# Kernel optimization log

Measured on AMD Instinct MI355X. Metric: run time of the kernel, lower is better.

## Reference

```python
import jax, jax.numpy as jnp
import numpy as np

B, S, H = 1, 1024, 2048
NH, NKV, HD = 32, 4, 128
E, K, I = 32, 8, 768
EPS = 1e-06
ROPE_BASE = 1e6


def rmsnorm(x, w, eps=EPS):
    xf = x.astype(jnp.float32)
    var = jnp.mean(xf * xf, axis=-1, keepdims=True)
    return w * (xf * jax.lax.rsqrt(var + eps)).astype(x.dtype)


def apply_rope(x, cos, sin):
    # x: [B,S,N,HD]; cos/sin: [S,HD//2]; interleaved (llama-style) pair rotation
    xr = x.reshape(*x.shape[:-1], HD // 2, 2)
    x0, x1 = xr[..., 0], xr[..., 1]
    c = cos[None, :, None, :]
    s = sin[None, :, None, :]
    o0 = x0 * c - x1 * s
    o1 = x0 * s + x1 * c
    return jnp.stack([o0, o1], axis=-1).reshape(x.shape)


def setup_inputs() -> dict:
    key = jax.random.key(0)
    ks = jax.random.split(key, 16)
    hidden_states = jax.random.normal(ks[0], (B, S, H), dtype=jnp.float32)
    # RoPE angles: positions * inv_freq  -> [S, HD//2]
    inv_freq = 1.0 / (ROPE_BASE ** (np.arange(0, HD, 2, dtype=np.float32) / HD))
    position_embeddings = jnp.asarray(np.arange(S, dtype=np.float32)[:, None] * inv_freq[None, :])
    # causal additive mask [1,1,S,S]
    causal = jnp.tril(jnp.ones((S, S), dtype=bool))
    attention_mask = jnp.where(causal, 0.0, -1e9).astype(jnp.float32)[None, None]
    w = 0.02
    params = {
        'ln1_w': jnp.ones((H,), jnp.float32),
        'ln2_w': jnp.ones((H,), jnp.float32),
        'q_w': w * jax.random.normal(ks[1], (H, NH * HD), jnp.float32),
        'k_w': w * jax.random.normal(ks[2], (H, NKV * HD), jnp.float32),
        'v_w': w * jax.random.normal(ks[3], (H, NKV * HD), jnp.float32),
        'o_w': w * jax.random.normal(ks[4], (NH * HD, H), jnp.float32),
        'qn_w': jnp.ones((HD,), jnp.float32),
        'kn_w': jnp.ones((HD,), jnp.float32),
        'gate_w': w * jax.random.normal(ks[5], (H, E), jnp.float32),
        'wg': w * jax.random.normal(ks[6], (E, H, I), jnp.float32),
        'wu': w * jax.random.normal(ks[7], (E, H, I), jnp.float32),
        'wd': w * jax.random.normal(ks[8], (E, I, H), jnp.float32),
    }
    return {'hidden_states': hidden_states, 'position_embeddings': position_embeddings,
            'attention_mask': attention_mask, 'start_pos': 0, **params}


def reference(hidden_states, position_embeddings, attention_mask, start_pos,
              ln1_w, ln2_w, q_w, k_w, v_w, o_w, qn_w, kn_w, gate_w, wg, wu, wd):
    x = hidden_states  # [B,S,H]
    # --- attention ---
    h = rmsnorm(x, ln1_w)
    q = rmsnorm((h @ q_w).reshape(B, S, NH, HD), qn_w)
    k = rmsnorm((h @ k_w).reshape(B, S, NKV, HD), kn_w)
    v = (h @ v_w).reshape(B, S, NKV, HD)
    cos, sin = jnp.cos(position_embeddings), jnp.sin(position_embeddings)
    q = apply_rope(q, cos, sin)
    k = apply_rope(k, cos, sin)
    q = q.transpose(0, 2, 1, 3)  # [B,NH,S,HD]
    k = jnp.repeat(k.transpose(0, 2, 1, 3), NH // NKV, axis=1)
    v = jnp.repeat(v.transpose(0, 2, 1, 3), NH // NKV, axis=1)
    scores = jnp.einsum('bhqd,bhkd->bhqk', q, k) * (HD ** -0.5) + attention_mask
    attn = jax.nn.softmax(scores, axis=-1)
    o = jnp.einsum('bhqk,bhkd->bhqd', attn, v).transpose(0, 2, 1, 3).reshape(B, S, NH * HD)
    x = x + o @ o_w
    # --- MoE ---
    h = rmsnorm(x, ln2_w).reshape(B * S, H)  # [T,H]
    probs = jax.nn.softmax((h @ gate_w).astype(jnp.float32), axis=-1)
    rw, sel = jax.lax.top_k(probs, K)  # [T,K]
    rw = rw / jnp.sum(rw, axis=-1, keepdims=True)  # norm_topk_prob
    T = B * S
    # dense combine weights [T,E]; zero for unselected experts (same math as loop)
    wte = jnp.zeros((T, E), jnp.float32).at[jnp.arange(T)[:, None], sel].add(rw).astype(h.dtype)
    g = jnp.einsum('th,ehi->tei', h, wg)
    u = jnp.einsum('th,ehi->tei', h, wu)
    act = jax.nn.silu(g) * u  # [T,E,I]
    moe = jnp.einsum('te,tei,eih->th', wte, act, wd)
    return x + moe.reshape(B, S, H)
```

## Files before the change

kernel.cpp:

```cpp
#include <hip/hip_runtime.h>
#include <hip/hip_bf16.h>

#define S_ 1024
#define H_ 2048
#define NH_ 32
#define NKV_ 4
#define HD_ 128
#define NE_ 32
#define TOPK_ 8
#define I_ 768
#define EPS_ 1e-6f
#define QS_ 5120
#define BK2 32
#define NPAR 4

typedef __bf16 bf16_t;
typedef __bf16 bf16x4v __attribute__((ext_vector_type(4)));
typedef __bf16 bf16x8 __attribute__((ext_vector_type(8)));
typedef float f32x4 __attribute__((ext_vector_type(4)));
typedef float f32x16 __attribute__((ext_vector_type(16)));
typedef unsigned short u16_t;
typedef unsigned int uint2v __attribute__((ext_vector_type(2)));
typedef unsigned int uint4v __attribute__((ext_vector_type(4)));

static __device__ __forceinline__ u16_t f2u(float x) {
  return __builtin_bit_cast(u16_t, (__bf16)x);
}
static __device__ __forceinline__ float u2f(u16_t u) {
  return (float)__builtin_bit_cast(__bf16, u);
}

static __device__ __forceinline__ void gload16(const bf16_t* g, bf16_t* l) {
  __builtin_amdgcn_global_load_lds(
      (const __attribute__((address_space(1))) unsigned int*)g,
      (__attribute__((address_space(3))) unsigned int*)l, 16, 0, 0);
}

template <bool WF32>
__global__ __launch_bounds__(256) void rmsnorm2_k(const float* __restrict__ x,
                                                  const float* __restrict__ w,
                                                  float* __restrict__ outf,
                                                  bf16_t* __restrict__ outb) {
  int r = blockIdx.x, tid = threadIdx.x;
  const float* xr = x + (size_t)r * H_;
  f32x4 a = *(const f32x4*)(xr + tid * 8);
  f32x4 b = *(const f32x4*)(xr + tid * 8 + 4);
  float ss = 0.f;
#pragma unroll
  for (int i = 0; i < 4; ++i) ss += a[i] * a[i] + b[i] * b[i];
#pragma unroll
  for (int m = 1; m < 64; m <<= 1) ss += __shfl_xor(ss, m);
  __shared__ float wsum[4];
  if ((tid & 63) == 0) wsum[tid >> 6] = ss;
  __syncthreads();
  ss = wsum[0] + wsum[1] + wsum[2] + wsum[3];
  float inv = rsqrtf(ss * (1.0f / H_) + EPS_);
  f32x4 w0 = *(const f32x4*)(w + tid * 8);
  f32x4 w1 = *(const f32x4*)(w + tid * 8 + 4);
  f32x4 o0, o1;
#pragma unroll
  for (int i = 0; i < 4; ++i) { o0[i] = a[i] * inv * w0[i]; o1[i] = b[i] * inv * w1[i]; }
  if constexpr (WF32) {
    *(f32x4*)(outf + (size_t)r * H_ + tid * 8) = o0;
    *(f32x4*)(outf + (size_t)r * H_ + tid * 8 + 4) = o1;
  }
  bf16x8 ob;
#pragma unroll
  for (int i = 0; i < 4; ++i) { ob[i] = (__bf16)o0[i]; ob[i + 4] = (__bf16)o1[i]; }
  *(bf16x8*)(outb + (size_t)r * H_ + tid * 8) = ob;
}

__global__ __launch_bounds__(256) void transp2_k(const float* __restrict__ in,
                                                 bf16_t* __restrict__ out, int R, int C) {
  __shared__ float tile[64][65];
  size_t zin = (size_t)blockIdx.z * R * C;
  int tx = threadIdx.x & 15, ty = threadIdx.x >> 4;
  int r0 = blockIdx.y * 64, c0 = blockIdx.x * 64;
#pragma unroll
  for (int i = 0; i < 4; ++i) {
    f32x4 v = *(const f32x4*)(in + zin + (size_t)(r0 + ty + i * 16) * C + c0 + tx * 4);
    tile[ty + i * 16][tx * 4 + 0] = v[0];
    tile[ty + i * 16][tx * 4 + 1] = v[1];
    tile[ty + i * 16][tx * 4 + 2] = v[2];
    tile[ty + i * 16][tx * 4 + 3] = v[3];
  }
  __syncthreads();
#pragma unroll
  for (int i = 0; i < 4; ++i) {
    int oc = ty + i * 16;
    bf16x4v o;
#pragma unroll
    for (int j = 0; j < 4; ++j) o[j] = (bf16_t)tile[tx * 4 + j][oc];
    *(bf16x4v*)(out + zin + (size_t)(c0 + oc) * R + r0 + tx * 4) = o;
  }
}

template <int BMT, int BNT, int WM, int WN, typename TC, bool RESID>
__global__ __launch_bounds__(512) void gemmd_k(
    const bf16_t* __restrict__ A, const bf16_t* __restrict__ Bt,
    const float* __restrict__ resid, TC* __restrict__ C, int M, int N, int K) {
  constexpr int MI = BMT / WM / 16;
  constexpr int NI = BNT / WN / 16;
  constexpr int ALW = BMT / 16 / 8;
  constexpr int NBL = BNT / 16;
  static_assert(NBL <= 8, "B wave loads");
  __shared__ __align__(16) bf16_t As[2][BMT][BK2];
  __shared__ __align__(16) bf16_t Bs[2][BNT][BK2];
  int tid = threadIdx.x, lane = tid & 63, w = tid >> 6;
  int m0 = blockIdx.x * BMT, n0 = blockIdx.y * BNT;
  int srow = lane >> 2;
  int schunk = ((lane & 3) ^ ((lane >> 3) & 3)) * 8;
  const bf16_t* asrc[ALW];
#pragma unroll
  for (int i = 0; i < ALW; ++i) {
    int r = (w * ALW + i) * 16 + srow;
    asrc[i] = A + (size_t)(m0 + r) * K + schunk;
  }
  bool hasB = (w < NBL);
  int brow = w * 16;
  const bf16_t* bsrc = hasB ? Bt + (size_t)(n0 + brow + srow) * K + schunk : nullptr;

  int fr = lane & 15, g = lane >> 4;
  int rk = (g ^ ((fr >> 1) & 3)) * 8;
  int wm = w / WN, wn = w % WN;
  int rbase0 = wm * (BMT / WM), cbase0 = wn * (BNT / WN);
  f32x4 acc[MI][NI] = {};
  int NT = K / BK2;
  {
#pragma unroll
    for (int i = 0; i < ALW; ++i) gload16(asrc[i], &As[0][(w * ALW + i) * 16][0]);
    if (hasB) gload16(bsrc, &Bs[0][brow][0]);
  }
  __syncthreads();
  int cur = 0;
  for (int t = 0; t < NT; ++t) {
    if (t + 1 < NT) {
      int ko = (t + 1) * BK2;
#pragma unroll
      for (int i = 0; i < ALW; ++i) gload16(asrc[i] + ko, &As[cur ^ 1][(w * ALW + i) * 16][0]);
      if (hasB) gload16(bsrc + ko, &Bs[cur ^ 1][brow][0]);
    }
    bf16x8 af[MI], bf[NI];
#pragma unroll
    for (int i = 0; i < MI; ++i) af[i] = *(const bf16x8*)&As[cur][rbase0 + i * 16 + fr][rk];
#pragma unroll
    for (int i = 0; i < NI; ++i) bf[i] = *(const bf16x8*)&Bs[cur][cbase0 + i * 16 + fr][rk];
#pragma unroll
    for (int mi = 0; mi < MI; ++mi)
#pragma unroll
      for (int ni = 0; ni < NI; ++ni)
        acc[mi][ni] = __builtin_amdgcn_mfma_f32_16x16x32_bf16(af[mi], bf[ni], acc[mi][ni], 0, 0, 0);
    __syncthreads();
    cur ^= 1;
  }
  int rbase = g * 4;
#pragma unroll
  for (int mi = 0; mi < MI; ++mi)
#pragma unroll
    for (int ni = 0; ni < NI; ++ni)
#pragma unroll
      for (int r = 0; r < 4; ++r) {
        int gi = m0 + rbase0 + mi * 16 + rbase + r;
        int gc = n0 + cbase0 + ni * 16 + fr;
        float v = acc[mi][ni][r];
        if constexpr (RESID) v += resid[(size_t)gi * N + gc];
        C[(size_t)gi * N + gc] = (TC)v;
      }
}

template <int BMT, int BNT, int WM, int WN, typename TC, bool GATHER, bool SCALE, bool DUAL>
__global__ __launch_bounds__(512) void gemme_k(
    const bf16_t* __restrict__ A, const bf16_t* __restrict__ B1g,
    const bf16_t* __restrict__ B2g, TC* __restrict__ C, bf16_t* __restrict__ act,
    const float* __restrict__ wlist, const int* __restrict__ counts,
    const int* __restrict__ offsets, const int* __restrict__ toklist,
    const int* __restrict__ mslots, const int* __restrict__ meta,
    int* __restrict__ qhead, int NTN, int N, int K) {
  constexpr int MI = BMT / WM / 16;
  constexpr int NI = BNT / WN / 16;
  constexpr int BNTT = BNT * (DUAL ? 2 : 1);
  constexpr int ALW = BMT / 16 / 8;
  constexpr int NBL = BNTT / 16;
  static_assert(NBL <= 8, "B wave loads");
  __shared__ __align__(16) bf16_t As[2][BMT][BK2];
  __shared__ __align__(16) bf16_t Bs[2][BNTT][BK2];
  __shared__ int s_w;
  int tid = threadIdx.x, lane = tid & 63, w = tid >> 6;
  int srow = lane >> 2;
  int schunk = ((lane & 3) ^ ((lane >> 3) & 3)) * 8;
  int fr = lane & 15, g = lane >> 4;
  int rk = (g ^ ((fr >> 1) & 3)) * 8;
  int wm = w / WN, wn = w % WN;
  int rbase0 = wm * (BMT / WM), cbase0 = wn * (BNT / WN);
  int total = meta[0] * NTN;
  for (;;) {
    if (tid == 0) s_w = atomicAdd(qhead, 1);
    __syncthreads();
    int wk = s_w;
    if (wk >= total) return;
    int ms = mslots[wk / NTN];
    int n0 = (wk % NTN) * BNT;
    int e = ms >> 8, m0 = (ms & 255) * BMT;
    int cnt = counts[e], off = offsets[e];
    size_t bs = (size_t)K * N;
    const bf16_t* B1 = B1g + (size_t)e * bs;
    const bf16_t* B2 = DUAL ? (B2g + (size_t)e * bs) : nullptr;
    const bf16_t* asrc[ALW];
#pragma unroll
    for (int i = 0; i < ALW; ++i) {
      int r = (w * ALW + i) * 16 + srow;
      int gr = min(m0 + r, cnt - 1);
      size_t grow;
      if constexpr (GATHER) grow = (size_t)toklist[e * S_ + gr];
      else grow = (size_t)(off + gr);
      asrc[i] = A + grow * (size_t)K + schunk;
    }
    bool hasB = (w < NBL);
    const bf16_t* bsrc = nullptr;
    int brow = w * 16;
    if (hasB) {
      const bf16_t* Bb = (brow < BNT) ? B1 : B2;
      int rr = (brow < BNT) ? brow : brow - BNT;
      bsrc = Bb + (size_t)(n0 + rr + srow) * K + schunk;
    }
    f32x4 acc1[MI][NI] = {};
    f32x4 acc2[DUAL ? MI : 1][DUAL ? NI : 1] = {};
    int NT = K / BK2;
    {
#pragma unroll
      for (int i = 0; i < ALW; ++i) gload16(asrc[i], &As[0][(w * ALW + i) * 16][0]);
      if (hasB) gload16(bsrc, &Bs[0][brow][0]);
    }
    __syncthreads();
    int cur = 0;
    for (int t = 0; t < NT; ++t) {
      if (t + 1 < NT) {
        int ko = (t + 1) * BK2;
#pragma unroll
        for (int i = 0; i < ALW; ++i) gload16(asrc[i] + ko, &As[cur ^ 1][(w * ALW + i) * 16][0]);
        if (hasB) gload16(bsrc + ko, &Bs[cur ^ 1][brow][0]);
      }
      bf16x8 af[MI], b1f[NI], b2f[DUAL ? NI : 1];
#pragma unroll
      for (int i = 0; i < MI; ++i) af[i] = *(const bf16x8*)&As[cur][rbase0 + i * 16 + fr][rk];
#pragma unroll
      for (int i = 0; i < NI; ++i) b1f[i] = *(const bf16x8*)&Bs[cur][cbase0 + i * 16 + fr][rk];
      if constexpr (DUAL) {
#pragma unroll
        for (int i = 0; i < NI; ++i) b2f[i] = *(const bf16x8*)&Bs[cur][BNT + cbase0 + i * 16 + fr][rk];
      }
#pragma unroll
      for (int mi = 0; mi < MI; ++mi)
#pragma unroll
        for (int ni = 0; ni < NI; ++ni) {
          acc1[mi][ni] = __builtin_amdgcn_mfma_f32_16x16x32_bf16(af[mi], b1f[ni], acc1[mi][ni], 0, 0, 0);
          if constexpr (DUAL)
            acc2[mi][ni] = __builtin_amdgcn_mfma_f32_16x16x32_bf16(af[mi], b2f[ni], acc2[mi][ni], 0, 0, 0);
        }
      __syncthreads();
      cur ^= 1;
    }
    int rbase = g * 4;
#pragma unroll
    for (int mi = 0; mi < MI; ++mi)
#pragma unroll
      for (int ni = 0; ni < NI; ++ni)
#pragma unroll
        for (int r = 0; r < 4; ++r) {
          int lr = rbase0 + mi * 16 + rbase + r;
          int gi = m0 + lr;
          if (gi >= cnt) continue;
          int gc = n0 + cbase0 + ni * 16 + fr;
          if constexpr (DUAL) {
            float gv = acc1[mi][ni][r], uv = acc2[mi][ni][r];
            float sig = 1.0f / (1.0f + __expf(-gv));
            act[(size_t)(off + gi) * N + gc] = (bf16_t)(gv * sig * uv);
          } else {
            float v = acc1[mi][ni][r];
            if constexpr (SCALE) v *= wlist[(size_t)e * S_ + gi];
            C[(size_t)(off + gi) * N + gc] = (TC)v;
          }
        }
  }
}

__global__ __launch_bounds__(64) void qkpack_k(const float* __restrict__ qkv,
                                               const float* __restrict__ qn,
                                               const float* __restrict__ kn,
                                               const float* __restrict__ pe,
                                               bf16_t* __restrict__ Q2,
                                               bf16_t* __restrict__ K2) {
  int s = blockIdx.x, hh = blockIdx.y, lane = threadIdx.x;
  const float* ptr;
  const float* w;
  if (hh < NH_) { ptr = qkv + (size_t)s * QS_ + hh * HD_; w = qn; }
  else          { ptr = qkv + (size_t)s * QS_ + NH_ * HD_ + (hh - NH_) * HD_; w = kn; }
  float x0 = ptr[2 * lane], x1 = ptr[2 * lane + 1];
  float ss = x0 * x0 + x1 * x1;
#pragma unroll
  for (int m = 1; m < 64; m <<= 1) ss += __shfl_xor(ss, m);
  float inv = rsqrtf(ss * (1.0f / HD_) + EPS_);
  x0 = x0 * inv * w[2 * lane];
  x1 = x1 * inv * w[2 * lane + 1];
  float ang = pe[(size_t)s * (HD_ / 2) + lane];
  float sn, cs;
  sincosf(ang, &sn, &cs);
  float r0 = x0 * cs - x1 * sn;
  float r1 = x0 * sn + x1 * cs;
  if (hh < NH_) {
    const float scale = 0.08838834764831845f;
    float a = r0 * scale, b = r1 * scale;
    u16_t h0 = f2u(a), h1 = f2u(b);
    unsigned hw = (unsigned)h0 | ((unsigned)h1 << 16);
    unsigned lw = (unsigned)f2u(a - u2f(h0)) | ((unsigned)f2u(b - u2f(h1)) << 16);
    unsigned* base = (unsigned*)(Q2 + ((size_t)s * NH_ + hh) * 256);
    base[lane] = hw;
    base[64 + lane] = lw;
  } else {
    u16_t h0 = f2u(r0), h1 = f2u(r1);
    unsigned hw = (unsigned)h0 | ((unsigned)h1 << 16);
    unsigned lw = (unsigned)f2u(r0 - u2f(h0)) | ((unsigned)f2u(r1 - u2f(h1)) << 16);
    int j = lane >> 2, off = (2 * lane) & 7;
    unsigned* base = (unsigned*)(K2 + ((size_t)(hh - NH_) * S_ + s) * 256);
    base[(((j) ^ (s & 31)) * 8 + off) >> 1] = hw;
    base[(((16 + j) ^ (s & 31)) * 8 + off) >> 1] = lw;
  }
}

__global__ __launch_bounds__(256) void vpack_k(const float* __restrict__ qkv,
                                               bf16_t* __restrict__ V2T) {
  int t = blockIdx.x, kvh = blockIdx.y;
  int kv0 = t * 64;
  bf16_t* dst = V2T + (size_t)(kvh * 16 + t) * 128 * 128;
  const float* vbase = qkv + NH_ * HD_ + NKV_ * HD_ + kvh * HD_;
#pragma unroll
  for (int i = 0; i < 4; ++i) {
    int flat = threadIdx.x + i * 256;
    int kvp = flat >> 5, d4 = (flat & 31) * 4;
    const float* r0 = vbase + (size_t)(kv0 + 2 * kvp) * QS_ + d4;
    const float* r1 = r0 + QS_;
    f32x4 a = *(const f32x4*)r0;
    f32x4 b = *(const f32x4*)r1;
    int kvg = (2 * kvp) >> 3, sub = (2 * kvp) & 7;
#pragma unroll
    for (int e = 0; e < 4; ++e) {
      int d = d4 + e;
      int fsw = (d ^ (d >> 4)) & 15;
      u16_t ha = f2u(a[e]), hb = f2u(b[e]);
      unsigned hw = (unsigned)ha | ((unsigned)hb << 16);
      unsigned lw = (unsigned)f2u(a[e] - u2f(ha)) | ((unsigned)f2u(b[e] - u2f(hb)) << 16);
      unsigned* dd = (unsigned*)(dst + d * 128);
      dd[((kvg ^ fsw) * 8 + sub) >> 1] = hw;
      dd[(((8 + kvg) ^ fsw) * 8 + sub) >> 1] = lw;
    }
  }
}

#define AKV 64
__global__ __launch_bounds__(512, 4) void attn5_k(const bf16_t* __restrict__ Q2,
                                                  const bf16_t* __restrict__ K2,
                                                  const bf16_t* __restrict__ V2T,
                                                  float* __restrict__ Op,
                                                  float* __restrict__ mlp) {
  int q0 = blockIdx.x * 32;
  int kvh = blockIdx.y;
  int par = blockIdx.z;
  int tid = threadIdx.x, lane = tid & 63, w = tid >> 6;
  int g = lane >> 5, c32 = lane & 31;
  int h = kvh * 8 + w;
  int qrow = q0 + c32;
  int last_t = (q0 + 31) >> 6;
  float2* mlv = (float2*)mlp;
  if (par > last_t) {
    if (g == 0) {
      float2 v2; v2.x = -3.0e38f; v2.y = 0.f;
      mlv[((size_t)par * S_ + qrow) * NH_ + h] = v2;
    }
    return;
  }
  __shared__ __align__(16) u16_t Kl[AKV * 256];
  __shared__ __align__(16) u16_t Vl[128 * 128];

  bf16x8 qh[8], ql[8];
  {
    const bf16_t* qp2 = Q2 + ((size_t)qrow * NH_ + h) * 256;
#pragma unroll
    for (int ks = 0; ks < 8; ++ks) {
      qh[ks] = *(const bf16x8*)(qp2 + g * 8 + ks * 16);
      ql[ks] = *(const bf16x8*)(qp2 + 128 + g * 8 + ks * 16);
    }
  }

  f32x16 accO[4] = {};
  float m = -3.0e38f, l = 0.f;

  for (int t = par; t <= last_t; t += NPAR) {
    int kv0 = t * AKV;
    __syncthreads();
    {
      const bf16_t* ksrc = K2 + ((size_t)kvh * S_ + kv0) * 256;
#pragma unroll
      for (int i = 0; i < 4; ++i) {
        int cbase = w * 64 + i * 512;
        gload16(ksrc + (size_t)(cbase + lane) * 8, (bf16_t*)&Kl[cbase * 8]);
      }
    }
    {
      const bf16_t* vsrc = V2T + (size_t)(kvh * 16 + t) * 128 * 128;
#pragma unroll
      for (int i = 0; i < 4; ++i) {
        int cbase = w * 64 + i * 512;
        gload16(vsrc + (size_t)(cbase + lane) * 8, (bf16_t*)&Vl[cbase * 8]);
      }
    }
    __syncthreads();

    f32x16 accS[2] = {};
#pragma unroll
    for (int ks = 0; ks < 8; ++ks) {
      int db = g * 8 + ks * 16;
#pragma unroll
      for (int mf = 0; mf < 2; ++mf) {
        int kvr = c32 + mf * 32;
        bf16x8 ah = *(const bf16x8*)&Kl[kvr * 256 + (((db >> 3)) ^ c32) * 8];
        bf16x8 al = *(const bf16x8*)&Kl[kvr * 256 + ((16 + (db >> 3)) ^ c32) * 8];
        accS[mf] = __builtin_amdgcn_mfma_f32_32x32x16_bf16(ah, qh[ks], accS[mf], 0, 0, 0);
        accS[mf] = __builtin_amdgcn_mfma_f32_32x32x16_bf16(ah, ql[ks], accS[mf], 0, 0, 0);
        accS[mf] = __builtin_amdgcn_mfma_f32_32x32x16_bf16(al, qh[ks], accS[mf], 0, 0, 0);
      }
    }
    float p[2][16];
    float tmax = -3.0e38f;
#pragma unroll
    for (int mf = 0; mf < 2; ++mf)
#pragma unroll
      for (int r = 0; r < 16; ++r) {
        int kvg = kv0 + mf * 32 + (r & 3) + 8 * (r >> 2) + 4 * g;
        float s = (kvg <= qrow) ? accS[mf][r] : -3.0e38f;
        p[mf][r] = s;
        tmax = fmaxf(tmax, s);
      }
    tmax = fmaxf(tmax, __shfl_xor(tmax, 32));
    float mn = fmaxf(m, tmax);
    float sc = __expf(m - mn);
    float ts = 0.f;
#pragma unroll
    for (int mf = 0; mf < 2; ++mf)
#pragma unroll
      for (int r = 0; r < 16; ++r) {
        float e = __expf(p[mf][r] - mn);
        p[mf][r] = e;
        ts += e;
      }
    ts += __shfl_xor(ts, 32);
    l = l * sc + ts;
    m = mn;
#pragma unroll
    for (int r = 0; r < 16; ++r) {
      int row16 = (r & 3) + 8 * (r >> 2) + 4 * g;
      float scr = __shfl(sc, row16);
#pragma unroll
      for (int nf = 0; nf < 4; ++nf) accO[nf][r] *= scr;
    }
#pragma unroll
    for (int ks = 0; ks < 4; ++ks) {
      int k1 = ks & 1, mf = ks >> 1;
      unsigned Lh[4], Ll[4];
#pragma unroll
      for (int i = 0; i < 4; ++i) {
        float a = p[mf][8 * k1 + 2 * i], b = p[mf][8 * k1 + 2 * i + 1];
        u16_t ha = f2u(a), hb = f2u(b);
        Lh[i] = (unsigned)ha | ((unsigned)hb << 16);
        Ll[i] = (unsigned)f2u(a - u2f(ha)) | ((unsigned)f2u(b - u2f(hb)) << 16);
      }
      unsigned Xh[4], Xl[4];
#pragma unroll
      for (int i = 0; i < 4; ++i) {
        Xh[i] = (unsigned)__shfl_xor((int)Lh[i], 32);
        Xl[i] = (unsigned)__shfl_xor((int)Ll[i], 32);
      }
      uint4v fh, fl;
      fh[0] = g ? Xh[2] : Lh[0]; fh[1] = g ? Xh[3] : Lh[1];
      fh[2] = g ? Lh[2] : Xh[0]; fh[3] = g ? Lh[3] : Xh[1];
      fl[0] = g ? Xl[2] : Ll[0]; fl[1] = g ? Xl[3] : Ll[1];
      fl[2] = g ? Ll[2] : Xl[0]; fl[3] = g ? Ll[3] : Xl[1];
      bf16x8 pH = __builtin_bit_cast(bf16x8, fh);
      bf16x8 pL = __builtin_bit_cast(bf16x8, fl);
      int kvb = g * 8 + ks * 16;
#pragma unroll
      for (int nf = 0; nf < 4; ++nf) {
        int d = c32 + nf * 32;
        int fsw = (d ^ (d >> 4)) & 15;
        bf16x8 vh = *(const bf16x8*)&Vl[d * 128 + (((kvb >> 3)) ^ fsw) * 8];
        bf16x8 vl = *(const bf16x8*)&Vl[d * 128 + ((8 + (kvb >> 3)) ^ fsw) * 8];
        accO[nf] = __builtin_amdgcn_mfma_f32_32x32x16_bf16(pH, vh, accO[nf], 0, 0, 0);
        accO[nf] = __builtin_amdgcn_mfma_f32_32x32x16_bf16(pH, vl, accO[nf], 0, 0, 0);
        accO[nf] = __builtin_amdgcn_mfma_f32_32x32x16_bf16(pL, vh, accO[nf], 0, 0, 0);
      }
    }
  }
#pragma unroll
  for (int r = 0; r < 16; ++r) {
    int row16 = (r & 3) + 8 * (r >> 2) + 4 * g;
    int orow = q0 + row16;
#pragma unroll
    for (int nf = 0; nf < 4; ++nf)
      __builtin_nontemporal_store(
          accO[nf][r], &Op[(((size_t)par * S_ + orow) * NH_ + h) * HD_ + nf * 32 + c32]);
  }
  if (g == 0) {
    float2 v2; v2.x = m; v2.y = l;
    mlv[((size_t)par * S_ + qrow) * NH_ + h] = v2;
  }
}

__global__ __launch_bounds__(128) void attnmerge_k(const float* __restrict__ Op,
                                                   const float* __restrict__ mlp,
                                                   bf16_t* __restrict__ o) {
  int row = blockIdx.x, h = blockIdx.y, d = threadIdx.x;
  const float2* mlv = (const float2*)mlp;
  float mm[NPAR], ll[NPAR];
  float M = -3.0e38f;
#pragma unroll
  for (int p = 0; p < NPAR; ++p) {
    float2 v2 = mlv[((size_t)p * S_ + row) * NH_ + h];
    mm[p] = v2.x; ll[p] = v2.y;
    M = fmaxf(M, mm[p]);
  }
  float acc = 0.f, L = 0.f;
#pragma unroll
  for (int p = 0; p < NPAR; ++p) {
    if (ll[p] == 0.f) continue;
    float wp = __expf(mm[p] - M);
    acc += wp * __builtin_nontemporal_load(
                    &Op[(((size_t)p * S_ + row) * NH_ + h) * HD_ + d]);
    L += wp * ll[p];
  }
  o[((size_t)row * NH_ + h) * HD_ + d] = (bf16_t)(acc / L);
}

__global__ __launch_bounds__(256) void router2_k(const float* __restrict__ h2,
                                                 const float* __restrict__ gw,
                                                 int* __restrict__ sel,
                                                 float* __restrict__ wsel) {
  int t = blockIdx.x, tid = threadIdx.x;
  int e = tid & 31, grp = tid >> 5;
  float acc = 0.f;
  for (int kk = grp; kk < H_; kk += 8)
    acc += h2[(size_t)t * H_ + kk] * gw[(size_t)kk * NE_ + e];
  __shared__ float part[8][32];
  part[grp][e] = acc;
  __syncthreads();
  if (tid < 64) {
    int lane = tid;
    float lg = -3.0e38f;
    if (lane < 32) {
      lg = 0.f;
      for (int g = 0; g < 8; ++g) lg += part[g][lane];
    }
    float tm = lg;
#pragma unroll
    for (int mm = 1; mm < 32; mm <<= 1) tm = fmaxf(tm, __shfl_xor(tm, mm));
    if (lane < 32) lg = __expf(lg - tm);
    bool avail = (lane < 32);
    float tot = 0.f;
    int se[TOPK_]; float rw[TOPK_];
#pragma unroll
    for (int kk = 0; kk < TOPK_; ++kk) {
      float val = avail ? lg : -1.f;
      float best = val;
#pragma unroll
      for (int mm = 1; mm < 32; mm <<= 1) best = fmaxf(best, __shfl_xor(best, mm));
      unsigned long long ball = __ballot(avail && (val == best));
      int bi = (int)__builtin_ctzll(ball);
      if (lane == bi) avail = false;
      se[kk] = bi;
      rw[kk] = best;
      tot += best;
    }
    float itot = 1.0f / tot;
    if (lane == 0) {
#pragma unroll
      for (int kk = 0; kk < TOPK_; ++kk) {
        sel[t * TOPK_ + kk] = se[kk];
        wsel[t * TOPK_ + kk] = rw[kk] * itot;
      }
    }
  }
}

__global__ __launch_bounds__(64) void build_k(const int* __restrict__ sel,
                                              const float* __restrict__ wsel,
                                              int* __restrict__ counts,
                                              int* __restrict__ toklist,
                                              float* __restrict__ wlist,
                                              int* __restrict__ pos) {
  int e = blockIdx.x, lane = threadIdx.x;
  int base = 0;
  for (int c = 0; c < S_ / 64; ++c) {
    int t = c * 64 + lane;
    int match = -1;
#pragma unroll
    for (int k = 0; k < TOPK_; ++k)
      if (sel[t * TOPK_ + k] == e) match = k;
    bool flag = (match >= 0);
    unsigned long long mask = __ballot(flag);
    int prefix = __popcll(mask & ((1ull << lane) - 1ull));
    if (flag) {
      int p = base + prefix;
      toklist[e * S_ + p] = t;
      wlist[e * S_ + p] = wsel[t * TOPK_ + match];
      pos[t * TOPK_ + match] = p;
    }
    base += __popcll(mask);
  }
  if (lane == 0) counts[e] = base;
}

__global__ void scan_k(const int* __restrict__ counts, int* __restrict__ offsets,
                       int* __restrict__ mslots, int* __restrict__ meta,
                       int* __restrict__ qheads) {
  if (threadIdx.x == 0 && blockIdx.x == 0) {
    int o = 0, ns = 0;
    for (int e = 0; e < NE_; ++e) {
      offsets[e] = o;
      int c = counts[e];
      for (int m0 = 0; m0 < c; m0 += 128) mslots[ns++] = (e << 8) | (m0 >> 7);
      o += c;
    }
    offsets[NE_] = o;
    meta[0] = ns;
    qheads[0] = 0;
    qheads[1] = 0;
  }
}

__global__ __launch_bounds__(256) void combine_k(const float* __restrict__ x1,
                                                 const bf16_t* __restrict__ pairout,
                                                 const int* __restrict__ sel,
                                                 const int* __restrict__ pos,
                                                 const int* __restrict__ offsets,
                                                 float* __restrict__ out) {
  int t = blockIdx.x, tid = threadIdx.x;
  int slots[TOPK_];
#pragma unroll
  for (int kk = 0; kk < TOPK_; ++kk)
    slots[kk] = offsets[sel[t * TOPK_ + kk]] + pos[t * TOPK_ + kk];
  int c = tid * 8;
  f32x4 s0 = *(const f32x4*)(x1 + (size_t)t * H_ + c);
  f32x4 s1 = *(const f32x4*)(x1 + (size_t)t * H_ + c + 4);
#pragma unroll
  for (int kk = 0; kk < TOPK_; ++kk) {
    bf16x8 pv = *(const bf16x8*)(pairout + (size_t)slots[kk] * H_ + c);
#pragma unroll
    for (int i = 0; i < 4; ++i) { s0[i] += (float)pv[i]; s1[i] += (float)pv[i + 4]; }
  }
  *(f32x4*)(out + (size_t)t * H_ + c) = s0;
  *(f32x4*)(out + (size_t)t * H_ + c + 4) = s1;
}

extern "C" void kernel_launch(void* const* d_in, const int* in_sizes, int n_in,
                              void* d_out, int out_size, void* d_ws, size_t ws_size,
                              hipStream_t stream) {
  const float* hidden = (const float*)d_in[0];
  const float* pe     = (const float*)d_in[1];
  const float* ln1    = (const float*)d_in[4];
  const float* ln2    = (const float*)d_in[5];
  const float* q_w    = (const float*)d_in[6];
  const float* k_w    = (const float*)d_in[7];
  const float* v_w    = (const float*)d_in[8];
  const float* o_w    = (const float*)d_in[9];
  const float* qn     = (const float*)d_in[10];
  const float* kn     = (const float*)d_in[11];
  const float* gate_w = (const float*)d_in[12];
  const float* wg     = (const float*)d_in[13];
  const float* wu     = (const float*)d_in[14];
  const float* wd     = (const float*)d_in[15];
  float* out = (float*)d_out;

  char* p = (char*)d_ws;
  auto alloc = [&](size_t bytes) {
    char* r = p;
    p += (bytes + 255) & ~(size_t)255;
    return r;
  };
  bf16_t* h1b     = (bf16_t*)alloc((size_t)S_ * H_ * 2);
  float*  qkv     = (float*)alloc((size_t)S_ * QS_ * 4);
  bf16_t* Q2      = (bf16_t*)alloc((size_t)S_ * NH_ * 256 * 2);
  bf16_t* K2      = (bf16_t*)alloc((size_t)NKV_ * S_ * 256 * 2);
  bf16_t* V2T     = (bf16_t*)alloc((size_t)NKV_ * 16 * 128 * 128 * 2);
  bf16_t* aob     = (bf16_t*)alloc((size_t)S_ * NH_ * HD_ * 2);
  float*  x1      = (float*)alloc((size_t)S_ * H_ * 4);
  float*  h2      = (float*)alloc((size_t)S_ * H_ * 4);
  bf16_t* h2b     = (bf16_t*)alloc((size_t)S_ * H_ * 2);
  bf16_t* act     = (bf16_t*)alloc((size_t)S_ * TOPK_ * I_ * 2);
  bf16_t* po      = (bf16_t*)alloc((size_t)S_ * TOPK_ * H_ * 2);
  float*  Opart   = (float*)alloc((size_t)NPAR * S_ * NH_ * HD_ * 4);
  float*  mlpart  = (float*)alloc((size_t)NPAR * S_ * NH_ * 8);
  int*    counts  = (int*)alloc(NE_ * 4);
  int*    offs    = (int*)alloc((NE_ + 1) * 4);
  int*    toklist = (int*)alloc((size_t)NE_ * S_ * 4);
  float*  wlist   = (float*)alloc((size_t)NE_ * S_ * 4);
  int*    sel     = (int*)alloc((size_t)S_ * TOPK_ * 4);
  float*  wsel    = (float*)alloc((size_t)S_ * TOPK_ * 4);
  int*    pos     = (int*)alloc((size_t)S_ * TOPK_ * 4);
  int*    mslots  = (int*)alloc(256 * 4);
  int*    meta    = (int*)alloc(4);
  int*    qheads  = (int*)alloc(2 * 4);
  bf16_t* qkvT = (bf16_t*)alloc((size_t)QS_ * H_ * 2);
  bf16_t* owT  = (bf16_t*)alloc((size_t)(NH_ * HD_) * H_ * 2);
  bf16_t* wgT  = (bf16_t*)alloc((size_t)NE_ * H_ * I_ * 2);
  bf16_t* wuT  = (bf16_t*)alloc((size_t)NE_ * H_ * I_ * 2);
  bf16_t* wdT  = (bf16_t*)alloc((size_t)NE_ * I_ * H_ * 2);
  bf16_t* qwTp = qkvT;
  bf16_t* kwTp = qkvT + (size_t)(NH_ * HD_) * H_;
  bf16_t* vwTp = qkvT + (size_t)(NH_ * HD_ + NKV_ * HD_) * H_;

  transp2_k<<<dim3((NH_ * HD_) / 64, H_ / 64, 1), 256, 0, stream>>>(q_w, qwTp, H_, NH_ * HD_);
  transp2_k<<<dim3((NKV_ * HD_) / 64, H_ / 64, 1), 256, 0, stream>>>(k_w, kwTp, H_, NKV_ * HD_);
  transp2_k<<<dim3((NKV_ * HD_) / 64, H_ / 64, 1), 256, 0, stream>>>(v_w, vwTp, H_, NKV_ * HD_);
  transp2_k<<<dim3(H_ / 64, (NH_ * HD_) / 64, 1), 256, 0, stream>>>(o_w, owT, NH_ * HD_, H_);
  transp2_k<<<dim3(I_ / 64, H_ / 64, NE_), 256, 0, stream>>>(wg, wgT, H_, I_);
  transp2_k<<<dim3(I_ / 64, H_ / 64, NE_), 256, 0, stream>>>(wu, wuT, H_, I_);
  transp2_k<<<dim3(H_ / 64, I_ / 64, NE_), 256, 0, stream>>>(wd, wdT, I_, H_);

  rmsnorm2_k<false><<<S_, 256, 0, stream>>>(hidden, ln1, nullptr, h1b);
  gemmd_k<128, 128, 2, 4, float, false>
      <<<dim3(S_ / 128, QS_ / 128), 512, 0, stream>>>(h1b, qkvT, nullptr, qkv, S_, QS_, H_);
  qkpack_k<<<dim3(S_, NH_ + NKV_), 64, 0, stream>>>(qkv, qn, kn, pe, Q2, K2);
  vpack_k<<<dim3(16, NKV_), 256, 0, stream>>>(qkv, V2T);
  attn5_k<<<dim3(S_ / 32, NKV_, NPAR), 512, 0, stream>>>(Q2, K2, V2T, Opart, mlpart);
  attnmerge_k<<<dim3(S_, NH_), 128, 0, stream>>>(Opart, mlpart, aob);
  gemmd_k<128, 128, 2, 4, float, true>
      <<<dim3(S_ / 128, H_ / 128), 512, 0, stream>>>(aob, owT, hidden, x1, S_, H_, NH_ * HD_);
  rmsnorm2_k<true><<<S_, 256, 0, stream>>>(x1, ln2, h2, h2b);
  router2_k<<<S_, 256, 0, stream>>>(h2, gate_w, sel, wsel);
  build_k<<<NE_, 64, 0, stream>>>(sel, wsel, counts, toklist, wlist, pos);
  scan_k<<<1, 64, 0, stream>>>(counts, offs, mslots, meta, qheads);
  gemme_k<128, 64, 4, 2, float, true, false, true>
      <<<1024, 512, 0, stream>>>(h2b, wgT, wuT, nullptr, act, wlist, counts, offs, toklist,
                                 mslots, meta, &qheads[0], I_ / 64, I_, H_);
  gemme_k<128, 128, 2, 4, bf16_t, false, true, false>
      <<<1024, 512, 0, stream>>>(act, wdT, nullptr, po, nullptr, wlist, counts, offs, nullptr,
                                 mslots, meta, &qheads[1], H_ / 128, H_, I_);
  combine_k<<<S_, 256, 0, stream>>>(x1, po, sel, pos, offs, out);
}
```

Baseline: 825.2 us.

## Pre-tile transposed weights into contiguous 16x32 blocks for GEMM B loads

The weight transpose kernel now writes bf16 weights in a tiled layout where each 16-row by 32-k tile is a contiguous 1 KB block that already carries the LDS swizzle. The dense and expert GEMMs compute B source addresses from this layout, so each wave's B load per k-step reads one contiguous 1 KB span instead of 16 rows strided by K. This is meant to improve coalescing and cut TLB and row overhead on the weight stream. It ties the GEMMs to K being a multiple of 32 and the transpose to this tiled format.

```diff
diff --git a/kernel.cpp b/kernel.cpp
--- a/kernel.cpp
+++ b/kernel.cpp
@@ -36,6 +36,10 @@
       (__attribute__((address_space(3))) unsigned int*)l, 16, 0, 0);
 }
 
+static __device__ __forceinline__ int tile_lane_off(int lane) {
+  return (lane >> 2) * 32 + (((lane & 3) ^ ((lane >> 3) & 3)) << 3);
+}
+
 template <bool WF32>
 __global__ __launch_bounds__(256) void rmsnorm2_k(const float* __restrict__ x,
                                                   const float* __restrict__ w,
@@ -70,29 +74,36 @@
   *(bf16x8*)(outb + (size_t)r * H_ + tid * 8) = ob;
 }
 
-__global__ __launch_bounds__(256) void transp2_k(const float* __restrict__ in,
+__global__ __launch_bounds__(256) void transp3_k(const float* __restrict__ in,
                                                  bf16_t* __restrict__ out, int R, int C) {
   __shared__ float tile[64][65];
-  size_t zin = (size_t)blockIdx.z * R * C;
+  size_t z = (size_t)blockIdx.z * R * C;
   int tx = threadIdx.x & 15, ty = threadIdx.x >> 4;
   int r0 = blockIdx.y * 64, c0 = blockIdx.x * 64;
 #pragma unroll
   for (int i = 0; i < 4; ++i) {
-    f32x4 v = *(const f32x4*)(in + zin + (size_t)(r0 + ty + i * 16) * C + c0 + tx * 4);
+    f32x4 v = *(const f32x4*)(in + z + (size_t)(r0 + ty + i * 16) * C + c0 + tx * 4);
     tile[ty + i * 16][tx * 4 + 0] = v[0];
     tile[ty + i * 16][tx * 4 + 1] = v[1];
     tile[ty + i * 16][tx * 4 + 2] = v[2];
     tile[ty + i * 16][tx * 4 + 3] = v[3];
   }
   __syncthreads();
-#pragma unroll
-  for (int i = 0; i < 4; ++i) {
-    int oc = ty + i * 16;
-    bf16x4v o;
-#pragma unroll
-    for (int j = 0; j < 4; ++j) o[j] = (bf16_t)tile[tx * 4 + j][oc];
-    *(bf16x4v*)(out + zin + (size_t)(c0 + oc) * R + r0 + tx * 4) = o;
-  }
+  int KT = R >> 5;
+  int flat = threadIdx.x * 16;
+  int lt = flat >> 9;
+  int within = flat & 511;
+  int nr = within >> 5;
+  int kc = within & 31;
+  int tn = lt >> 1, tk = lt & 1;
+  bf16x8 o0, o1;
+#pragma unroll
+  for (int j = 0; j < 8; ++j) o0[j] = (bf16_t)tile[tk * 32 + kc + j][tn * 16 + nr];
+#pragma unroll
+  for (int j = 0; j < 8; ++j) o1[j] = (bf16_t)tile[tk * 32 + kc + 8 + j][tn * 16 + nr];
+  size_t tidx = ((size_t)((c0 >> 4) + tn) * KT + (r0 >> 5) + tk) << 9;
+  *(bf16x8*)(out + z + tidx + nr * 32 + kc) = o0;
+  *(bf16x8*)(out + z + tidx + nr * 32 + kc + 8) = o1;
 }
 
 template <int BMT, int BNT, int WM, int WN, typename TC, bool RESID>
@@ -118,7 +129,9 @@
   }
   bool hasB = (w < NBL);
   int brow = w * 16;
-  const bf16_t* bsrc = hasB ? Bt + (size_t)(n0 + brow + srow) * K + schunk : nullptr;
+  const bf16_t* bsrc = nullptr;
+  if (hasB)
+    bsrc = Bt + ((size_t)((n0 + brow) >> 4) * (K >> 5)) * 512 + tile_lane_off(lane);
 
   int fr = lane & 15, g = lane >> 4;
   int rk = (g ^ ((fr >> 1) & 3)) * 8;
@@ -138,7 +151,7 @@
       int ko = (t + 1) * BK2;
 #pragma unroll
       for (int i = 0; i < ALW; ++i) gload16(asrc[i] + ko, &As[cur ^ 1][(w * ALW + i) * 16][0]);
-      if (hasB) gload16(bsrc + ko, &Bs[cur ^ 1][brow][0]);
+      if (hasB) gload16(bsrc + (size_t)(t + 1) * 512, &Bs[cur ^ 1][brow][0]);
     }
     bf16x8 af[MI], bf[NI];
 #pragma unroll
@@ -188,10 +201,12 @@
   int tid = threadIdx.x, lane = tid & 63, w = tid >> 6;
   int srow = lane >> 2;
   int schunk = ((lane & 3) ^ ((lane >> 3) & 3)) * 8;
+  int tloff = tile_lane_off(lane);
   int fr = lane & 15, g = lane >> 4;
   int rk = (g ^ ((fr >> 1) & 3)) * 8;
   int wm = w / WN, wn = w % WN;
   int rbase0 = wm * (BMT / WM), cbase0 = wn * (BNT / WN);
+  int KT = K >> 5;
   int total = meta[0] * NTN;
   for (;;) {
     if (tid == 0) s_w = atomicAdd(qhead, 1);
@@ -221,7 +236,7 @@
     if (hasB) {
       const bf16_t* Bb = (brow < BNT) ? B1 : B2;
       int rr = (brow < BNT) ? brow : brow - BNT;
-      bsrc = Bb + (size_t)(n0 + rr + srow) * K + schunk;
+      bsrc = Bb + ((size_t)((n0 + rr) >> 4) * KT) * 512 + tloff;
     }
     f32x4 acc1[MI][NI] = {};
     f32x4 acc2[DUAL ? MI : 1][DUAL ? NI : 1] = {};
@@ -238,7 +253,7 @@
         int ko = (t + 1) * BK2;
 #pragma unroll
         for (int i = 0; i < ALW; ++i) gload16(asrc[i] + ko, &As[cur ^ 1][(w * ALW + i) * 16][0]);
-        if (hasB) gload16(bsrc + ko, &Bs[cur ^ 1][brow][0]);
+        if (hasB) gload16(bsrc + (size_t)(t + 1) * 512, &Bs[cur ^ 1][brow][0]);
       }
       bf16x8 af[MI], b1f[NI], b2f[DUAL ? NI : 1];
 #pragma unroll
@@ -716,13 +731,13 @@
   bf16_t* kwTp = qkvT + (size_t)(NH_ * HD_) * H_;
   bf16_t* vwTp = qkvT + (size_t)(NH_ * HD_ + NKV_ * HD_) * H_;
 
-  transp2_k<<<dim3((NH_ * HD_) / 64, H_ / 64, 1), 256, 0, stream>>>(q_w, qwTp, H_, NH_ * HD_);
-  transp2_k<<<dim3((NKV_ * HD_) / 64, H_ / 64, 1), 256, 0, stream>>>(k_w, kwTp, H_, NKV_ * HD_);
-  transp2_k<<<dim3((NKV_ * HD_) / 64, H_ / 64, 1), 256, 0, stream>>>(v_w, vwTp, H_, NKV_ * HD_);
-  transp2_k<<<dim3(H_ / 64, (NH_ * HD_) / 64, 1), 256, 0, stream>>>(o_w, owT, NH_ * HD_, H_);
-  transp2_k<<<dim3(I_ / 64, H_ / 64, NE_), 256, 0, stream>>>(wg, wgT, H_, I_);
-  transp2_k<<<dim3(I_ / 64, H_ / 64, NE_), 256, 0, stream>>>(wu, wuT, H_, I_);
-  transp2_k<<<dim3(H_ / 64, I_ / 64, NE_), 256, 0, stream>>>(wd, wdT, I_, H_);
+  transp3_k<<<dim3((NH_ * HD_) / 64, H_ / 64, 1), 256, 0, stream>>>(q_w, qwTp, H_, NH_ * HD_);
+  transp3_k<<<dim3((NKV_ * HD_) / 64, H_ / 64, 1), 256, 0, stream>>>(k_w, kwTp, H_, NKV_ * HD_);
+  transp3_k<<<dim3((NKV_ * HD_) / 64, H_ / 64, 1), 256, 0, stream>>>(v_w, vwTp, H_, NKV_ * HD_);
+  transp3_k<<<dim3(H_ / 64, (NH_ * HD_) / 64, 1), 256, 0, stream>>>(o_w, owT, NH_ * HD_, H_);
+  transp3_k<<<dim3(I_ / 64, H_ / 64, NE_), 256, 0, stream>>>(wg, wgT, H_, I_);
+  transp3_k<<<dim3(I_ / 64, H_ / 64, NE_), 256, 0, stream>>>(wu, wuT, H_, I_);
+  transp3_k<<<dim3(H_ / 64, I_ / 64, NE_), 256, 0, stream>>>(wd, wdT, I_, H_);
 
   rmsnorm2_k<false><<<S_, 256, 0, stream>>>(hidden, ln1, nullptr, h1b);
   gemmd_k<128, 128, 2, 4, float, false>
```

After: 842.8 us. +2.1%, slower.
